# Performance work log

Hardware: AMD Instinct MI355X
Metric: run time of the kernel (lower is better)

## Reference

```python
import jax, jax.numpy as jnp
import numpy as np
from jax import lax

N_FFT = 512
HOP = 128
Q = N_FFT // HOP  # 4
KW = 2 * N_FFT - 1  # conv kernel width 1023


def _hann_periodic(n: int) -> np.ndarray:
    # scipy.signal.get_window('hann', n) default fftbins=True -> periodic hann
    k = np.arange(n)
    return (0.5 - 0.5 * np.cos(2.0 * np.pi * k / n)).astype(np.float64)


def _compute_alpha(W: np.ndarray, S: np.ndarray) -> np.ndarray:
    # Faithful port of ConsistencyLoss._compute_alpha (paper eq. 9)
    N, R = N_FFT, HOP
    alpha = np.zeros((2 * Q - 1, 2 * N - 1), dtype=np.complex64)
    for qi, q in enumerate(range(-(Q - 1), Q)):
        S_sh = np.zeros(N)
        s0, s1 = max(0, -q * R), min(N, N - q * R)
        if s0 < s1:
            S_sh[s0:s1] = S[q * R + s0: q * R + s1]
        term = W * S_sh
        f = np.fft.fft(term, 2 * N - 1)
        alpha[qi] = np.fft.fftshift(f) / N
    alpha[Q - 1, N - 1] -= 1.0
    return alpha


def setup_inputs() -> dict:
    key = jax.random.key(0)
    waveform = 0.1 * jax.random.normal(key, (4, 131072), dtype=jnp.float32)
    W_np = _hann_periodic(N_FFT)
    alpha = _compute_alpha(W_np, W_np)
    return {
        "waveform": waveform,
        "window": jnp.asarray(W_np, dtype=jnp.float32),
        "alpha_real": jnp.asarray(alpha.real, dtype=jnp.float32),
        "alpha_imag": jnp.asarray(alpha.imag, dtype=jnp.float32),
    }


def _stft(waveform, window):
    # torch.stft(center=True, pad_mode='reflect', onesided=True), output (B, T, F)
    N, hop = N_FFT, HOP
    B, L = waveform.shape
    padded = jnp.pad(waveform, ((0, 0), (N // 2, N // 2)), mode="reflect")
    T = 1 + L // hop
    idx = hop * jnp.arange(T)[:, None] + jnp.arange(N)[None, :]  # (T, N)
    frames = padded[:, idx] * window  # (B, T, N)
    return jnp.fft.rfft(frames, axis=-1)  # (B, T, N//2+1) complex64


def reference(waveform, window, alpha_real, alpha_imag):
    N, hop = N_FFT, HOP
    B = waveform.shape[0]
    H = _stft(waveform, window)  # (B, T, N//2+1)
    T = H.shape[1]

    # reconstruct full two-sided spectrum: concat conj-flipped interior bins
    H_full = jnp.concatenate([H, jnp.conj(H[:, :, 1:-1][:, :, ::-1])], axis=2)  # (B, T, N)
    H_full = jnp.transpose(H_full, (0, 2, 1))  # (B, N, T)

    # fuse the phase-term einsum into the per-frequency conv kernel:
    # C[b,n,t] = sum_q phase[n,q] * (alpha[q] * H_full[b,n])(t)
    #          = (K_eff[n] * H_full[b,n])(t),  K_eff = phase @ alpha
    q_idx = jnp.arange(-(Q - 1), Q, dtype=jnp.float32)
    n_idx = jnp.arange(N, dtype=jnp.float32)
    phase = jnp.exp(1j * (2.0 * jnp.pi / N) * n_idx[:, None] * q_idx[None, :])  # (N, 2Q-1)
    alpha = alpha_real + 1j * alpha_imag  # (2Q-1, KW)
    K = phase @ alpha.astype(jnp.complex64)  # (N, KW)
    Kr, Ki = jnp.real(K), jnp.imag(K)

    # complex depthwise (groups=N) cross-correlation via real 2-channel trick
    Hri = jnp.stack([jnp.real(H_full), jnp.imag(H_full)], axis=2).reshape(B, 2 * N, T)
    kern = jnp.stack([
        jnp.stack([Kr, -Ki], axis=1),  # real output rows (N, 2, KW)
        jnp.stack([Ki, Kr], axis=1),   # imag output rows (N, 2, KW)
    ], axis=1).reshape(2 * N, 2, KW)
    out = lax.conv_general_dilated(
        Hri, kern, window_strides=(1,), padding=[(N - 1, N - 1)],
        dimension_numbers=("NCH", "OIH", "NCH"), feature_group_count=N,
    )  # (B, 2N, T)
    Cr, Ci = out[:, 0::2], out[:, 1::2]  # (B, N, T)

    loss = jnp.sum(Cr * Cr + Ci * Ci)
    return loss / (B * T)
```

## Files before the change

kernel.cpp:

```cpp
#include <hip/hip_runtime.h>
#include <math.h>

#define T_FRAMES 1025
#define TSTRIDE  1032
#define BATCH    4
#define LWAV     131072
#define KWC      1023
#define MFFT     2048
#define PI_F     3.14159265358979323846f

struct c32 { float r, i; };
__device__ __forceinline__ c32 mkc(float r, float i){ c32 z; z.r=r; z.i=i; return z; }
__device__ __forceinline__ c32 cadd(c32 a, c32 b){ return mkc(a.r+b.r, a.i+b.i); }
__device__ __forceinline__ c32 csub(c32 a, c32 b){ return mkc(a.r-b.r, a.i-b.i); }
__device__ __forceinline__ c32 cmul(c32 a, c32 b){ return mkc(a.r*b.r - a.i*b.i, a.r*b.i + a.i*b.r); }
__device__ __forceinline__ c32 cni(c32 a){ return mkc(a.i, -a.r); }
#define C8F 0.70710678118654752440f
__device__ __forceinline__ c32 c8p(c32 a){ return mkc(C8F*(a.r+a.i), C8F*(a.i-a.r)); }
__device__ __forceinline__ c32 c8m(c32 a){ return mkc(C8F*(a.i-a.r), -C8F*(a.r+a.i)); }

__device__ __forceinline__ void st2(float2* X, int p, c32 v){ X[p] = make_float2(v.r, v.i); }
__device__ __forceinline__ c32 ld2(const float2* X, int p){ float2 e = X[p]; return mkc(e.x, e.y); }

__device__ __forceinline__ int pX(int j){ return j + (j >> 5); }
__device__ __forceinline__ int pS2(int j){ return j + (j >> 4); }
__device__ __forceinline__ int rev9(int j){ return (int)(__brev((unsigned)j) >> 23); }

__device__ __forceinline__ c32 wexp(int r) {
    float s, c;
    __sincosf((float)r * (-PI_F / 1024.0f), &s, &c);
    return mkc(c, s);
}

__device__ __forceinline__ void dif8_tw(c32 y[8], c32 w3) {
    c32 w2 = cmul(w3, w3), w1 = cmul(w2, w2);
    c32 u[8], v[8], d;
    d = csub(y[0], y[4]); u[0] = cadd(y[0], y[4]); u[4] = cmul(d, w3);
    d = csub(y[1], y[5]); u[1] = cadd(y[1], y[5]); u[5] = c8p(cmul(d, w3));
    d = csub(y[2], y[6]); u[2] = cadd(y[2], y[6]); u[6] = cni(cmul(d, w3));
    d = csub(y[3], y[7]); u[3] = cadd(y[3], y[7]); u[7] = c8m(cmul(d, w3));
    d = csub(u[0], u[2]); v[0] = cadd(u[0], u[2]); v[2] = cmul(d, w2);
    d = csub(u[1], u[3]); v[1] = cadd(u[1], u[3]); v[3] = cni(cmul(d, w2));
    d = csub(u[4], u[6]); v[4] = cadd(u[4], u[6]); v[6] = cmul(d, w2);
    d = csub(u[5], u[7]); v[5] = cadd(u[5], u[7]); v[7] = cni(cmul(d, w2));
    d = csub(v[0], v[1]); y[0] = cadd(v[0], v[1]); y[1] = cmul(d, w1);
    d = csub(v[2], v[3]); y[2] = cadd(v[2], v[3]); y[3] = cmul(d, w1);
    d = csub(v[4], v[5]); y[4] = cadd(v[4], v[5]); y[5] = cmul(d, w1);
    d = csub(v[6], v[7]); y[6] = cadd(v[6], v[7]); y[7] = cmul(d, w1);
}
__device__ __forceinline__ void dif8_nt(c32 y[8]) {
    c32 u[8], v[8], d;
    d = csub(y[0], y[4]); u[0] = cadd(y[0], y[4]); u[4] = d;
    d = csub(y[1], y[5]); u[1] = cadd(y[1], y[5]); u[5] = c8p(d);
    d = csub(y[2], y[6]); u[2] = cadd(y[2], y[6]); u[6] = cni(d);
    d = csub(y[3], y[7]); u[3] = cadd(y[3], y[7]); u[7] = c8m(d);
    d = csub(u[0], u[2]); v[0] = cadd(u[0], u[2]); v[2] = d;
    d = csub(u[1], u[3]); v[1] = cadd(u[1], u[3]); v[3] = cni(d);
    d = csub(u[4], u[6]); v[4] = cadd(u[4], u[6]); v[6] = d;
    d = csub(u[5], u[7]); v[5] = cadd(u[5], u[7]); v[7] = cni(d);
    d = csub(v[0], v[1]); y[0] = cadd(v[0], v[1]); y[1] = d;
    d = csub(v[2], v[3]); y[2] = cadd(v[2], v[3]); y[3] = d;
    d = csub(v[4], v[5]); y[4] = cadd(v[4], v[5]); y[5] = d;
    d = csub(v[6], v[7]); y[6] = cadd(v[6], v[7]); y[7] = d;
}
__device__ __forceinline__ void dit8_tw(c32 y[8], c32 w3) {
    c32 w2 = cmul(w3, w3), w1 = cmul(w2, w2);
    c32 u[8], v[8], t;
    t = cmul(y[1], w1); u[0] = cadd(y[0], t); u[1] = csub(y[0], t);
    t = cmul(y[3], w1); u[2] = cadd(y[2], t); u[3] = csub(y[2], t);
    t = cmul(y[5], w1); u[4] = cadd(y[4], t); u[5] = csub(y[4], t);
    t = cmul(y[7], w1); u[6] = cadd(y[6], t); u[7] = csub(y[6], t);
    t = cmul(u[2], w2);      v[0] = cadd(u[0], t); v[2] = csub(u[0], t);
    t = cni(cmul(u[3], w2)); v[1] = cadd(u[1], t); v[3] = csub(u[1], t);
    t = cmul(u[6], w2);      v[4] = cadd(u[4], t); v[6] = csub(u[4], t);
    t = cni(cmul(u[7], w2)); v[5] = cadd(u[5], t); v[7] = csub(u[5], t);
    t = cmul(v[4], w3);      y[0] = cadd(v[0], t); y[4] = csub(v[0], t);
    t = c8p(cmul(v[5], w3)); y[1] = cadd(v[1], t); y[5] = csub(v[1], t);
    t = cni(cmul(v[6], w3)); y[2] = cadd(v[2], t); y[6] = csub(v[2], t);
    t = c8m(cmul(v[7], w3)); y[3] = cadd(v[3], t); y[7] = csub(v[3], t);
}
__device__ __forceinline__ void dit8_nt(c32 y[8]) {
    c32 u[8], v[8], t;
    u[0] = cadd(y[0], y[1]); u[1] = csub(y[0], y[1]);
    u[2] = cadd(y[2], y[3]); u[3] = csub(y[2], y[3]);
    u[4] = cadd(y[4], y[5]); u[5] = csub(y[4], y[5]);
    u[6] = cadd(y[6], y[7]); u[7] = csub(y[6], y[7]);
    t = u[2];      v[0] = cadd(u[0], t); v[2] = csub(u[0], t);
    t = cni(u[3]); v[1] = cadd(u[1], t); v[3] = csub(u[1], t);
    t = u[6];      v[4] = cadd(u[4], t); v[6] = csub(u[4], t);
    t = cni(u[7]); v[5] = cadd(u[5], t); v[7] = csub(u[5], t);
    t = v[4];      y[0] = cadd(v[0], t); y[4] = csub(v[0], t);
    t = c8p(v[5]); y[1] = cadd(v[1], t); y[5] = csub(v[1], t);
    t = cni(v[6]); y[2] = cadd(v[2], t); y[6] = csub(v[2], t);
    t = c8m(v[7]); y[3] = cadd(v[3], t); y[7] = csub(v[3], t);
}
__device__ __forceinline__ void dif4(c32 y[4]) {
    c32 u0 = cadd(y[0], y[2]), d0 = csub(y[0], y[2]);
    c32 u1 = cadd(y[1], y[3]), d1 = cni(csub(y[1], y[3]));
    y[0] = cadd(u0, u1); y[1] = csub(u0, u1);
    y[2] = cadd(d0, d1); y[3] = csub(d0, d1);
}
__device__ __forceinline__ void dif4_tw(c32 y[4], c32 w) {
    c32 w2 = cmul(w, w), w3 = cmul(w2, w);
    c32 s0 = cadd(y[0], y[2]), d0 = csub(y[0], y[2]);
    c32 s1 = cadd(y[1], y[3]), d1 = cni(csub(y[1], y[3]));
    y[0] = cadd(s0, s1);
    y[1] = cmul(csub(s0, s1), w2);
    y[2] = cmul(cadd(d0, d1), w);
    y[3] = cmul(csub(d0, d1), w3);
}
__device__ __forceinline__ void dit4(c32 y[4], c32 w) {
    c32 w2 = cmul(w, w);
    c32 t1 = cmul(y[1], w2); c32 u0 = cadd(y[0], t1), u1 = csub(y[0], t1);
    c32 t3 = cmul(y[3], w2); c32 u2 = cadd(y[2], t3), u3 = csub(y[2], t3);
    c32 s2 = cmul(u2, w);      y[0] = cadd(u0, s2); y[2] = csub(u0, s2);
    c32 s3 = cni(cmul(u3, w)); y[1] = cadd(u1, s3); y[3] = csub(u1, s3);
}

#define FSTR 548
__global__ __launch_bounds__(256) void stage1_kernel(const float* __restrict__ wave,
                                                     const float* __restrict__ win,
                                                     const float* __restrict__ ar,
                                                     const float* __restrict__ ai,
                                                     float2* __restrict__ Ht,
                                                     float2* __restrict__ Afbr,
                                                     float* __restrict__ out) {
    __shared__ float2 S2[2192];
    const int tid = threadIdx.x;

    if (blockIdx.x >= 8) {
        float2* F = S2;
        const int bid = blockIdx.x - 8;
        const int w = tid >> 6, l = tid & 63;
        const int b = bid / 257;
        const int t0 = (bid - b * 257) << 2;
        const float* wb = wave + (size_t)b * LWAV;
        const int j = w;
        const int t = t0 + j;

#pragma unroll 1
        for (int rep = 0; rep < 2; ++rep) {
            if (t < T_FRAMES) {
                c32 y[8];
#pragma unroll
                for (int k = 0; k < 8; ++k) {
                    int s = l + (k << 6);
                    int posn = t * 128 + s - 256;
                    int ix = posn < 0 ? -posn : (posn >= LWAV ? 2 * LWAV - 2 - posn : posn);
                    y[k] = mkc(wb[ix] * win[s], 0.f);
                }
                dif8_tw(y, wexp(l << 2));
#pragma unroll
                for (int k = 0; k < 8; ++k) st2(F, j*FSTR + pS2(l + (k << 6)), y[k]);
                __builtin_amdgcn_wave_barrier();
                {
                    int base = ((l >> 3) << 6) + (l & 7);
#pragma unroll
                    for (int k = 0; k < 8; ++k) y[k] = ld2(F, j*FSTR + pS2(base + (k << 3)));
                    dif8_tw(y, wexp((l & 7) << 5));
#pragma unroll
                    for (int k = 0; k < 8; ++k) st2(F, j*FSTR + pS2(base + (k << 3)), y[k]);
                }
                __builtin_amdgcn_wave_barrier();
                {
#pragma unroll
                    for (int k = 0; k < 8; ++k) y[k] = ld2(F, j*FSTR + pS2((l << 3) + k));
                    dif8_nt(y);
#pragma unroll
                    for (int k = 0; k < 8; ++k) st2(F, j*FSTR + pS2((l << 3) + k), y[k]);
                }
            }
            __syncthreads();
            const int jj = tid & 3;
            const int rb = tid >> 2;
            if (t0 + jj < T_FRAMES) {
#pragma unroll
                for (int rr = 0; rr < 4; ++rr) {
                    int p = ((rr << 6) + rb) << 1;
                    Ht[(size_t)(b * 512 + p) * TSTRIDE + t0 + jj] = F[jj*FSTR + pS2(p)];
                }
                if (tid < 4)
                    Ht[(size_t)(b * 512 + 1) * TSTRIDE + t0 + jj] = F[jj*FSTR + pS2(1)];
            }
            __syncthreads();
        }
    } else if (blockIdx.x < 7) {
        float2* X = S2;
        const int q = blockIdx.x;
#pragma unroll 1
        for (int rep = 0; rep < 2; ++rep) {
            c32 y[8];
#pragma unroll
            for (int k = 0; k < 8; ++k) {
                int j = tid + (k << 8);
                y[k] = (j < KWC) ? mkc(ar[q * KWC + j], -ai[q * KWC + j]) : mkc(0.f, 0.f);
            }
            dif8_tw(y, wexp(tid));
#pragma unroll
            for (int k = 0; k < 8; ++k) st2(X, pX(tid + (k << 8)), y[k]);
            __syncthreads();
            {
                int base = ((tid >> 5) << 8) + (tid & 31);
#pragma unroll
                for (int k = 0; k < 8; ++k) y[k] = ld2(X, pX(base + (k << 5)));
                dif8_tw(y, wexp((tid & 31) << 3));
#pragma unroll
                for (int k = 0; k < 8; ++k) st2(X, pX(base + (k << 5)), y[k]);
            }
            __syncthreads();
            {
                int base = ((tid & 63) << 5) + (tid >> 6);
#pragma unroll
                for (int k = 0; k < 8; ++k) y[k] = ld2(X, pX(base + (k << 2)));
                dif8_tw(y, wexp((tid >> 6) << 6));
#pragma unroll
                for (int k = 0; k < 8; ++k) st2(X, pX(base + (k << 2)), y[k]);
            }
            __syncthreads();
#pragma unroll
            for (int h = 0; h < 2; ++h) {
                int g = tid + (h << 8);
                c32 z4[4];
#pragma unroll
                for (int k = 0; k < 4; ++k) z4[k] = ld2(X, pX((g << 2) + k));
                dif4(z4);
#pragma unroll
                for (int k = 0; k < 4; ++k) {
                    int jx = (g << 2) + k;
                    int j4 = jx >> 1, lo = jx & 1;
                    int wv4 = j4 >> 8, rem = j4 & 255;
                    int r = rem >> 5, c = (rem >> 2) & 7, kk = rem & 3;
                    int s = (wv4 << 8) | (kk << 6) | (r << 3) | c;
                    Afbr[(q << 11) + (s << 1) + lo] = make_float2(z4[k].r, -z4[k].i);
                }
            }
            __syncthreads();
        }
    } else {
        if (tid == 0) *out = 0.f;
    }
}

__global__ __launch_bounds__(256) void conv_kernel(const float2* __restrict__ Ht,
                                                   const float2* __restrict__ Afbr,
                                                   float* __restrict__ out) {
    __shared__ float2 S2[4224];
    __shared__ float red[4];
    const int tid = threadIdx.x;
    const int l = tid & 63, wv = tid >> 6;
    const int g = blockIdx.x;
    const int half = g / 257;
    const int n = g - half * 257;
    const int b0 = half << 1;
    const int pr = rev9(n);

    const c32 wA  = wexp(tid);
    const c32 wB  = wexp((l & 31) << 3);
    const c32 wP3 = wexp((l & 7) << 5);
    const c32 wI2 = wexp((l & 3) << 6);
    const c32 wg1B = c8p(wB);
    const c32 wg1I = c8p(wI2);
    const c32 p1 = wexp(-(n << 2));
    const c32 p2 = cmul(p1, p1);
    const c32 p3 = cmul(p2, p1);

    const int Bb   = (((wv << 1) + (l >> 5)) << 8) + (l & 31);
    const int chunk = wv << 9;
    const int p3b  = chunk + ((l >> 3) << 6) + (l & 7);
    const int pos0 = chunk + ((l >> 3) << 6) + ((l & 7) << 3);
    const int px0  = pX(pos0);
    const int i2b  = chunk + ((l >> 2) << 5) + (l & 3);
    const int i3b  = chunk + ((l >> 5) << 8) + (l & 31);
    const int abase = (wv << 8) + l;
    const float4* af4 = (const float4*)Afbr;

#pragma unroll 1
    for (int r = 0; r < 2; ++r) {
        const float2* row = Ht + (size_t)((b0 + r) * 512 + pr) * TSTRIDE;
        float2* X = S2 + r * 2112;
        c32 y[8];
#pragma unroll
        for (int k = 0; k < 4; ++k) { float2 h = row[tid + (k << 8)]; y[k] = mkc(h.x, h.y); }
        if (tid == 0) { float2 h = row[1024]; y[4] = mkc(h.x, h.y); } else y[4] = mkc(0.f, 0.f);
        y[5] = mkc(0.f, 0.f); y[6] = mkc(0.f, 0.f); y[7] = mkc(0.f, 0.f);
        dif8_tw(y, wA);
#pragma unroll
        for (int k = 0; k < 8; ++k) st2(X, pX(tid + (k << 8)), y[k]);
    }
    __syncthreads();

#pragma unroll 1
    for (int r = 0; r < 2; ++r) {
        float2* X = S2 + r * 2112;
        c32 y[8];
#pragma unroll
        for (int gg = 0; gg < 2; ++gg)
#pragma unroll
            for (int t = 0; t < 4; ++t) y[gg*4+t] = ld2(X, pX(Bb + (gg << 5) + (t << 6)));
        dif4_tw(&y[0], wB); dif4_tw(&y[4], wg1B);
#pragma unroll
        for (int gg = 0; gg < 2; ++gg)
#pragma unroll
            for (int t = 0; t < 4; ++t) st2(X, pX(Bb + (gg << 5) + (t << 6)), y[gg*4+t]);
    }
    __builtin_amdgcn_wave_barrier();

#pragma unroll 1
    for (int r = 0; r < 2; ++r) {
        float2* X = S2 + r * 2112;
        c32 y[8];
#pragma unroll
        for (int u = 0; u < 8; ++u) y[u] = ld2(X, pX(p3b + (u << 3)));
        dif8_tw(y, wP3);
#pragma unroll
        for (int u = 0; u < 8; ++u) st2(X, pX(p3b + (u << 3)), y[u]);
    }
    __builtin_amdgcn_wave_barrier();

#pragma unroll 1
    for (int r = 0; r < 2; ++r) {
        float2* X = S2 + r * 2112;
        c32 y[8];
#pragma unroll
        for (int u = 0; u < 8; ++u) y[u] = ld2(X, px0 + u);
        dif8_nt(y);
#pragma unroll
        for (int k = 0; k < 8; ++k) {
            const int kk = k >> 1;
            float4 a;
            c32 Kk;
            a = af4[(3 << 10) + abase + (kk << 6)];
            float ax = (k & 1) ? a.z : a.x, ay = (k & 1) ? a.w : a.y;
            Kk = mkc(ax, ay);
            a = af4[(4 << 10) + abase + (kk << 6)]; ax = (k & 1) ? a.z : a.x; ay = (k & 1) ? a.w : a.y;
            Kk.r += p1.r * ax - p1.i * ay;  Kk.i += p1.r * ay + p1.i * ax;
            a = af4[(2 << 10) + abase + (kk << 6)]; ax = (k & 1) ? a.z : a.x; ay = (k & 1) ? a.w : a.y;
            Kk.r += p1.r * ax + p1.i * ay;  Kk.i += p1.r * ay - p1.i * ax;
            a = af4[(5 << 10) + abase + (kk << 6)]; ax = (k & 1) ? a.z : a.x; ay = (k & 1) ? a.w : a.y;
            Kk.r += p2.r * ax - p2.i * ay;  Kk.i += p2.r * ay + p2.i * ax;
            a = af4[(1 << 10) + abase + (kk << 6)]; ax = (k & 1) ? a.z : a.x; ay = (k & 1) ? a.w : a.y;
            Kk.r += p2.r * ax + p2.i * ay;  Kk.i += p2.r * ay - p2.i * ax;
            a = af4[(6 << 10) + abase + (kk << 6)]; ax = (k & 1) ? a.z : a.x; ay = (k & 1) ? a.w : a.y;
            Kk.r += p3.r * ax - p3.i * ay;  Kk.i += p3.r * ay + p3.i * ax;
            a = af4[(0 << 10) + abase + (kk << 6)]; ax = (k & 1) ? a.z : a.x; ay = (k & 1) ? a.w : a.y;
            Kk.r += p3.r * ax + p3.i * ay;  Kk.i += p3.r * ay - p3.i * ax;
            c32 P = cmul(y[k], Kk);
            y[k] = mkc(P.r, -P.i);
        }
        dit8_nt(y);
#pragma unroll
        for (int u = 0; u < 8; ++u) st2(X, px0 + u, y[u]);
    }
    __builtin_amdgcn_wave_barrier();

#pragma unroll 1
    for (int r = 0; r < 2; ++r) {
        float2* X = S2 + r * 2112;
        c32 y[8];
#pragma unroll
        for (int gg = 0; gg < 2; ++gg)
#pragma unroll
            for (int t = 0; t < 4; ++t) y[gg*4+t] = ld2(X, pX(i2b + (gg << 2) + (t << 3)));
        dit4(&y[0], wI2); dit4(&y[4], wg1I);
#pragma unroll
        for (int gg = 0; gg < 2; ++gg)
#pragma unroll
            for (int t = 0; t < 4; ++t) st2(X, pX(i2b + (gg << 2) + (t << 3)), y[gg*4+t]);
    }
    __builtin_amdgcn_wave_barrier();

#pragma unroll 1
    for (int r = 0; r < 2; ++r) {
        float2* X = S2 + r * 2112;
        c32 y[8];
#pragma unroll
        for (int k = 0; k < 8; ++k) y[k] = ld2(X, pX(i3b + (k << 5)));
        dit8_tw(y, wB);
#pragma unroll
        for (int k = 0; k < 8; ++k) st2(X, pX(i3b + (k << 5)), y[k]);
    }
    __syncthreads();

    float local = 0.f;
#pragma unroll 1
    for (int r = 0; r < 2; ++r) {
        float2* X = S2 + r * 2112;
        c32 y[8];
#pragma unroll
        for (int k = 0; k < 8; ++k) y[k] = ld2(X, pX(tid + (k << 8)));
        dit8_tw(y, wA);
        local += y[0].r*y[0].r + y[0].i*y[0].i
               + y[1].r*y[1].r + y[1].i*y[1].i
               + y[7].r*y[7].r + y[7].i*y[7].i;
        if (tid < 2)  local += y[2].r*y[2].r + y[2].i*y[2].i;
        if (tid >= 1) local += y[6].r*y[6].r + y[6].i*y[6].i;
    }
    local *= (n == 0 || n == 256) ? 1.0f : 2.0f;
#pragma unroll
    for (int off = 32; off >= 1; off >>= 1) local += __shfl_down(local, off);
    if ((tid & 63) == 0) red[tid >> 6] = local;
    __syncthreads();
    if (tid == 0) {
        const float SCALE =
            (float)(1.0 / ((double)MFFT * (double)MFFT * (double)BATCH * (double)T_FRAMES));
        atomicAdd(out, (red[0] + red[1] + red[2] + red[3]) * SCALE);
    }
}

extern "C" void kernel_launch(void* const* d_in, const int* in_sizes, int n_in,
                              void* d_out, int out_size, void* d_ws, size_t ws_size,
                              hipStream_t stream) {
    (void)in_sizes; (void)n_in; (void)out_size; (void)ws_size;
    const float* wave   = (const float*)d_in[0];
    const float* window = (const float*)d_in[1];
    const float* ar     = (const float*)d_in[2];
    const float* ai     = (const float*)d_in[3];
    float* out = (float*)d_out;

    char* ws = (char*)d_ws;
    float2* Ht   = (float2*)ws;
    float2* Afbr = (float2*)(ws + 16908288);

    stage1_kernel<<<1036, 256, 0, stream>>>(wave, window, ar, ai, Ht, Afbr, out);
    conv_kernel<<<2 * 257, 256, 0, stream>>>(Ht, Afbr, out);
}
```

Measured before the change: 89.42 us.

## Drop duplicated stage1 repetition and give each conv block one batch row

The stage1 STFT and alpha-FFT paths each ran their whole body twice in a `rep` loop, repeating identical work; the loop is removed so each runs once. The conv kernel no longer processes two batch rows per block in a double-sized shared buffer. It now launches one block per (batch, frequency) pair, doubling the grid and halving shared memory per block to raise occupancy and parallelism. In exchange, per-block setup such as twiddle factors is repeated across more blocks.

New measurement: 88.04 us. Within noise of the previous version (-1.5%).

```diff
diff --git a/kernel.cpp b/kernel.cpp
--- a/kernel.cpp
+++ b/kernel.cpp
@@ -138,103 +138,95 @@
         const int j = w;
         const int t = t0 + j;
 
-#pragma unroll 1
-        for (int rep = 0; rep < 2; ++rep) {
-            if (t < T_FRAMES) {
-                c32 y[8];
-#pragma unroll
-                for (int k = 0; k < 8; ++k) {
-                    int s = l + (k << 6);
-                    int posn = t * 128 + s - 256;
-                    int ix = posn < 0 ? -posn : (posn >= LWAV ? 2 * LWAV - 2 - posn : posn);
-                    y[k] = mkc(wb[ix] * win[s], 0.f);
-                }
-                dif8_tw(y, wexp(l << 2));
-#pragma unroll
-                for (int k = 0; k < 8; ++k) st2(F, j*FSTR + pS2(l + (k << 6)), y[k]);
-                __builtin_amdgcn_wave_barrier();
-                {
-                    int base = ((l >> 3) << 6) + (l & 7);
-#pragma unroll
-                    for (int k = 0; k < 8; ++k) y[k] = ld2(F, j*FSTR + pS2(base + (k << 3)));
-                    dif8_tw(y, wexp((l & 7) << 5));
-#pragma unroll
-                    for (int k = 0; k < 8; ++k) st2(F, j*FSTR + pS2(base + (k << 3)), y[k]);
-                }
-                __builtin_amdgcn_wave_barrier();
-                {
-#pragma unroll
-                    for (int k = 0; k < 8; ++k) y[k] = ld2(F, j*FSTR + pS2((l << 3) + k));
-                    dif8_nt(y);
-#pragma unroll
-                    for (int k = 0; k < 8; ++k) st2(F, j*FSTR + pS2((l << 3) + k), y[k]);
-                }
-            }
-            __syncthreads();
-            const int jj = tid & 3;
-            const int rb = tid >> 2;
-            if (t0 + jj < T_FRAMES) {
-#pragma unroll
-                for (int rr = 0; rr < 4; ++rr) {
-                    int p = ((rr << 6) + rb) << 1;
-                    Ht[(size_t)(b * 512 + p) * TSTRIDE + t0 + jj] = F[jj*FSTR + pS2(p)];
-                }
-                if (tid < 4)
-                    Ht[(size_t)(b * 512 + 1) * TSTRIDE + t0 + jj] = F[jj*FSTR + pS2(1)];
-            }
-            __syncthreads();
+        if (t < T_FRAMES) {
+            c32 y[8];
+#pragma unroll
+            for (int k = 0; k < 8; ++k) {
+                int s = l + (k << 6);
+                int posn = t * 128 + s - 256;
+                int ix = posn < 0 ? -posn : (posn >= LWAV ? 2 * LWAV - 2 - posn : posn);
+                y[k] = mkc(wb[ix] * win[s], 0.f);
+            }
+            dif8_tw(y, wexp(l << 2));
+#pragma unroll
+            for (int k = 0; k < 8; ++k) st2(F, j*FSTR + pS2(l + (k << 6)), y[k]);
+            __builtin_amdgcn_wave_barrier();
+            {
+                int base = ((l >> 3) << 6) + (l & 7);
+#pragma unroll
+                for (int k = 0; k < 8; ++k) y[k] = ld2(F, j*FSTR + pS2(base + (k << 3)));
+                dif8_tw(y, wexp((l & 7) << 5));
+#pragma unroll
+                for (int k = 0; k < 8; ++k) st2(F, j*FSTR + pS2(base + (k << 3)), y[k]);
+            }
+            __builtin_amdgcn_wave_barrier();
+            {
+#pragma unroll
+                for (int k = 0; k < 8; ++k) y[k] = ld2(F, j*FSTR + pS2((l << 3) + k));
+                dif8_nt(y);
+#pragma unroll
+                for (int k = 0; k < 8; ++k) st2(F, j*FSTR + pS2((l << 3) + k), y[k]);
+            }
+        }
+        __syncthreads();
+        const int jj = tid & 3;
+        const int rb = tid >> 2;
+        if (t0 + jj < T_FRAMES) {
+#pragma unroll
+            for (int rr = 0; rr < 4; ++rr) {
+                int p = ((rr << 6) + rb) << 1;
+                Ht[(size_t)(b * 512 + p) * TSTRIDE + t0 + jj] = F[jj*FSTR + pS2(p)];
+            }
+            if (tid < 4)
+                Ht[(size_t)(b * 512 + 1) * TSTRIDE + t0 + jj] = F[jj*FSTR + pS2(1)];
         }
     } else if (blockIdx.x < 7) {
         float2* X = S2;
         const int q = blockIdx.x;
-#pragma unroll 1
-        for (int rep = 0; rep < 2; ++rep) {
-            c32 y[8];
-#pragma unroll
-            for (int k = 0; k < 8; ++k) {
-                int j = tid + (k << 8);
-                y[k] = (j < KWC) ? mkc(ar[q * KWC + j], -ai[q * KWC + j]) : mkc(0.f, 0.f);
-            }
-            dif8_tw(y, wexp(tid));
-#pragma unroll
-            for (int k = 0; k < 8; ++k) st2(X, pX(tid + (k << 8)), y[k]);
-            __syncthreads();
-            {
-                int base = ((tid >> 5) << 8) + (tid & 31);
-#pragma unroll
-                for (int k = 0; k < 8; ++k) y[k] = ld2(X, pX(base + (k << 5)));
-                dif8_tw(y, wexp((tid & 31) << 3));
-#pragma unroll
-                for (int k = 0; k < 8; ++k) st2(X, pX(base + (k << 5)), y[k]);
-            }
-            __syncthreads();
-            {
-                int base = ((tid & 63) << 5) + (tid >> 6);
-#pragma unroll
-                for (int k = 0; k < 8; ++k) y[k] = ld2(X, pX(base + (k << 2)));
-                dif8_tw(y, wexp((tid >> 6) << 6));
-#pragma unroll
-                for (int k = 0; k < 8; ++k) st2(X, pX(base + (k << 2)), y[k]);
-            }
-            __syncthreads();
-#pragma unroll
-            for (int h = 0; h < 2; ++h) {
-                int g = tid + (h << 8);
-                c32 z4[4];
-#pragma unroll
-                for (int k = 0; k < 4; ++k) z4[k] = ld2(X, pX((g << 2) + k));
-                dif4(z4);
-#pragma unroll
-                for (int k = 0; k < 4; ++k) {
-                    int jx = (g << 2) + k;
-                    int j4 = jx >> 1, lo = jx & 1;
-                    int wv4 = j4 >> 8, rem = j4 & 255;
-                    int r = rem >> 5, c = (rem >> 2) & 7, kk = rem & 3;
-                    int s = (wv4 << 8) | (kk << 6) | (r << 3) | c;
-                    Afbr[(q << 11) + (s << 1) + lo] = make_float2(z4[k].r, -z4[k].i);
-                }
-            }
-            __syncthreads();
+        c32 y[8];
+#pragma unroll
+        for (int k = 0; k < 8; ++k) {
+            int j = tid + (k << 8);
+            y[k] = (j < KWC) ? mkc(ar[q * KWC + j], -ai[q * KWC + j]) : mkc(0.f, 0.f);
+        }
+        dif8_tw(y, wexp(tid));
+#pragma unroll
+        for (int k = 0; k < 8; ++k) st2(X, pX(tid + (k << 8)), y[k]);
+        __syncthreads();
+        {
+            int base = ((tid >> 5) << 8) + (tid & 31);
+#pragma unroll
+            for (int k = 0; k < 8; ++k) y[k] = ld2(X, pX(base + (k << 5)));
+            dif8_tw(y, wexp((tid & 31) << 3));
+#pragma unroll
+            for (int k = 0; k < 8; ++k) st2(X, pX(base + (k << 5)), y[k]);
+        }
+        __syncthreads();
+        {
+            int base = ((tid & 63) << 5) + (tid >> 6);
+#pragma unroll
+            for (int k = 0; k < 8; ++k) y[k] = ld2(X, pX(base + (k << 2)));
+            dif8_tw(y, wexp((tid >> 6) << 6));
+#pragma unroll
+            for (int k = 0; k < 8; ++k) st2(X, pX(base + (k << 2)), y[k]);
+        }
+        __syncthreads();
+#pragma unroll
+        for (int h = 0; h < 2; ++h) {
+            int g = tid + (h << 8);
+            c32 z4[4];
+#pragma unroll
+            for (int k = 0; k < 4; ++k) z4[k] = ld2(X, pX((g << 2) + k));
+            dif4(z4);
+#pragma unroll
+            for (int k = 0; k < 4; ++k) {
+                int jx = (g << 2) + k;
+                int j4 = jx >> 1, lo = jx & 1;
+                int wv4 = j4 >> 8, rem = j4 & 255;
+                int r = rem >> 5, c = (rem >> 2) & 7, kk = rem & 3;
+                int s = (wv4 << 8) | (kk << 6) | (r << 3) | c;
+                Afbr[(q << 11) + (s << 1) + lo] = make_float2(z4[k].r, -z4[k].i);
+            }
         }
     } else {
         if (tid == 0) *out = 0.f;
@@ -244,15 +236,15 @@
 __global__ __launch_bounds__(256) void conv_kernel(const float2* __restrict__ Ht,
                                                    const float2* __restrict__ Afbr,
                                                    float* __restrict__ out) {
-    __shared__ float2 S2[4224];
+    __shared__ float2 X[2112];
     __shared__ float red[4];
     const int tid = threadIdx.x;
     const int l = tid & 63, wv = tid >> 6;
     const int g = blockIdx.x;
-    const int half = g / 257;
-    const int n = g - half * 257;
-    const int b0 = half << 1;
+    const int b = g / 257;
+    const int n = g - b * 257;
     const int pr = rev9(n);
+    const float2* row = Ht + (size_t)(b * 512 + pr) * TSTRIDE;
 
     const c32 wA  = wexp(tid);
     const c32 wB  = wexp((l & 31) << 3);
@@ -274,127 +266,92 @@
     const int abase = (wv << 8) + l;
     const float4* af4 = (const float4*)Afbr;
 
-#pragma unroll 1
-    for (int r = 0; r < 2; ++r) {
-        const float2* row = Ht + (size_t)((b0 + r) * 512 + pr) * TSTRIDE;
-        float2* X = S2 + r * 2112;
-        c32 y[8];
-#pragma unroll
-        for (int k = 0; k < 4; ++k) { float2 h = row[tid + (k << 8)]; y[k] = mkc(h.x, h.y); }
-        if (tid == 0) { float2 h = row[1024]; y[4] = mkc(h.x, h.y); } else y[4] = mkc(0.f, 0.f);
-        y[5] = mkc(0.f, 0.f); y[6] = mkc(0.f, 0.f); y[7] = mkc(0.f, 0.f);
-        dif8_tw(y, wA);
-#pragma unroll
-        for (int k = 0; k < 8; ++k) st2(X, pX(tid + (k << 8)), y[k]);
+    c32 y[8];
+#pragma unroll
+    for (int k = 0; k < 4; ++k) { float2 h = row[tid + (k << 8)]; y[k] = mkc(h.x, h.y); }
+    if (tid == 0) { float2 h = row[1024]; y[4] = mkc(h.x, h.y); } else y[4] = mkc(0.f, 0.f);
+    y[5] = mkc(0.f, 0.f); y[6] = mkc(0.f, 0.f); y[7] = mkc(0.f, 0.f);
+    dif8_tw(y, wA);
+#pragma unroll
+    for (int k = 0; k < 8; ++k) st2(X, pX(tid + (k << 8)), y[k]);
+    __syncthreads();
+
+#pragma unroll
+    for (int gg = 0; gg < 2; ++gg)
+#pragma unroll
+        for (int t = 0; t < 4; ++t) y[gg*4+t] = ld2(X, pX(Bb + (gg << 5) + (t << 6)));
+    dif4_tw(&y[0], wB); dif4_tw(&y[4], wg1B);
+#pragma unroll
+    for (int gg = 0; gg < 2; ++gg)
+#pragma unroll
+        for (int t = 0; t < 4; ++t) st2(X, pX(Bb + (gg << 5) + (t << 6)), y[gg*4+t]);
+    __builtin_amdgcn_wave_barrier();
+
+#pragma unroll
+    for (int u = 0; u < 8; ++u) y[u] = ld2(X, pX(p3b + (u << 3)));
+    dif8_tw(y, wP3);
+#pragma unroll
+    for (int u = 0; u < 8; ++u) st2(X, pX(p3b + (u << 3)), y[u]);
+    __builtin_amdgcn_wave_barrier();
+
+#pragma unroll
+    for (int u = 0; u < 8; ++u) y[u] = ld2(X, px0 + u);
+    dif8_nt(y);
+#pragma unroll
+    for (int k = 0; k < 8; ++k) {
+        const int kk = k >> 1;
+        float4 a;
+        c32 Kk;
+        a = af4[(3 << 10) + abase + (kk << 6)];
+        float ax = (k & 1) ? a.z : a.x, ay = (k & 1) ? a.w : a.y;
+        Kk = mkc(ax, ay);
+        a = af4[(4 << 10) + abase + (kk << 6)]; ax = (k & 1) ? a.z : a.x; ay = (k & 1) ? a.w : a.y;
+        Kk.r += p1.r * ax - p1.i * ay;  Kk.i += p1.r * ay + p1.i * ax;
+        a = af4[(2 << 10) + abase + (kk << 6)]; ax = (k & 1) ? a.z : a.x; ay = (k & 1) ? a.w : a.y;
+        Kk.r += p1.r * ax + p1.i * ay;  Kk.i += p1.r * ay - p1.i * ax;
+        a = af4[(5 << 10) + abase + (kk << 6)]; ax = (k & 1) ? a.z : a.x; ay = (k & 1) ? a.w : a.y;
+        Kk.r += p2.r * ax - p2.i * ay;  Kk.i += p2.r * ay + p2.i * ax;
+        a = af4[(1 << 10) + abase + (kk << 6)]; ax = (k & 1) ? a.z : a.x; ay = (k & 1) ? a.w : a.y;
+        Kk.r += p2.r * ax + p2.i * ay;  Kk.i += p2.r * ay - p2.i * ax;
+        a = af4[(6 << 10) + abase + (kk << 6)]; ax = (k & 1) ? a.z : a.x; ay = (k & 1) ? a.w : a.y;
+        Kk.r += p3.r * ax - p3.i * ay;  Kk.i += p3.r * ay + p3.i * ax;
+        a = af4[(0 << 10) + abase + (kk << 6)]; ax = (k & 1) ? a.z : a.x; ay = (k & 1) ? a.w : a.y;
+        Kk.r += p3.r * ax + p3.i * ay;  Kk.i += p3.r * ay - p3.i * ax;
+        c32 P = cmul(y[k], Kk);
+        y[k] = mkc(P.r, -P.i);
     }
+    dit8_nt(y);
+#pragma unroll
+    for (int u = 0; u < 8; ++u) st2(X, px0 + u, y[u]);
+    __builtin_amdgcn_wave_barrier();
+
+#pragma unroll
+    for (int gg = 0; gg < 2; ++gg)
+#pragma unroll
+        for (int t = 0; t < 4; ++t) y[gg*4+t] = ld2(X, pX(i2b + (gg << 2) + (t << 3)));
+    dit4(&y[0], wI2); dit4(&y[4], wg1I);
+#pragma unroll
+    for (int gg = 0; gg < 2; ++gg)
+#pragma unroll
+        for (int t = 0; t < 4; ++t) st2(X, pX(i2b + (gg << 2) + (t << 3)), y[gg*4+t]);
+    __builtin_amdgcn_wave_barrier();
+
+#pragma unroll
+    for (int k = 0; k < 8; ++k) y[k] = ld2(X, pX(i3b + (k << 5)));
+    dit8_tw(y, wB);
+#pragma unroll
+    for (int k = 0; k < 8; ++k) st2(X, pX(i3b + (k << 5)), y[k]);
     __syncthreads();
 
-#pragma unroll 1
-    for (int r = 0; r < 2; ++r) {
-        float2* X = S2 + r * 2112;
-        c32 y[8];
-#pragma unroll
-        for (int gg = 0; gg < 2; ++gg)
-#pragma unroll
-            for (int t = 0; t < 4; ++t) y[gg*4+t] = ld2(X, pX(Bb + (gg << 5) + (t << 6)));
-        dif4_tw(&y[0], wB); dif4_tw(&y[4], wg1B);
-#pragma unroll
-        for (int gg = 0; gg < 2; ++gg)
-#pragma unroll
-            for (int t = 0; t < 4; ++t) st2(X, pX(Bb + (gg << 5) + (t << 6)), y[gg*4+t]);
-    }
-    __builtin_amdgcn_wave_barrier();
-
-#pragma unroll 1
-    for (int r = 0; r < 2; ++r) {
-        float2* X = S2 + r * 2112;
-        c32 y[8];
-#pragma unroll
-        for (int u = 0; u < 8; ++u) y[u] = ld2(X, pX(p3b + (u << 3)));
-        dif8_tw(y, wP3);
-#pragma unroll
-        for (int u = 0; u < 8; ++u) st2(X, pX(p3b + (u << 3)), y[u]);
-    }
-    __builtin_amdgcn_wave_barrier();
-
-#pragma unroll 1
-    for (int r = 0; r < 2; ++r) {
-        float2* X = S2 + r * 2112;
-        c32 y[8];
-#pragma unroll
-        for (int u = 0; u < 8; ++u) y[u] = ld2(X, px0 + u);
-        dif8_nt(y);
-#pragma unroll
-        for (int k = 0; k < 8; ++k) {
-            const int kk = k >> 1;
-            float4 a;
-            c32 Kk;
-            a = af4[(3 << 10) + abase + (kk << 6)];
-            float ax = (k & 1) ? a.z : a.x, ay = (k & 1) ? a.w : a.y;
-            Kk = mkc(ax, ay);
-            a = af4[(4 << 10) + abase + (kk << 6)]; ax = (k & 1) ? a.z : a.x; ay = (k & 1) ? a.w : a.y;
-            Kk.r += p1.r * ax - p1.i * ay;  Kk.i += p1.r * ay + p1.i * ax;
-            a = af4[(2 << 10) + abase + (kk << 6)]; ax = (k & 1) ? a.z : a.x; ay = (k & 1) ? a.w : a.y;
-            Kk.r += p1.r * ax + p1.i * ay;  Kk.i += p1.r * ay - p1.i * ax;
-            a = af4[(5 << 10) + abase + (kk << 6)]; ax = (k & 1) ? a.z : a.x; ay = (k & 1) ? a.w : a.y;
-            Kk.r += p2.r * ax - p2.i * ay;  Kk.i += p2.r * ay + p2.i * ax;
-            a = af4[(1 << 10) + abase + (kk << 6)]; ax = (k & 1) ? a.z : a.x; ay = (k & 1) ? a.w : a.y;
-            Kk.r += p2.r * ax + p2.i * ay;  Kk.i += p2.r * ay - p2.i * ax;
-            a = af4[(6 << 10) + abase + (kk << 6)]; ax = (k & 1) ? a.z : a.x; ay = (k & 1) ? a.w : a.y;
-            Kk.r += p3.r * ax - p3.i * ay;  Kk.i += p3.r * ay + p3.i * ax;
-            a = af4[(0 << 10) + abase + (kk << 6)]; ax = (k & 1) ? a.z : a.x; ay = (k & 1) ? a.w : a.y;
-            Kk.r += p3.r * ax + p3.i * ay;  Kk.i += p3.r * ay - p3.i * ax;
-            c32 P = cmul(y[k], Kk);
-            y[k] = mkc(P.r, -P.i);
-        }
-        dit8_nt(y);
-#pragma unroll
-        for (int u = 0; u < 8; ++u) st2(X, px0 + u, y[u]);
-    }
-    __builtin_amdgcn_wave_barrier();
-
-#pragma unroll 1
-    for (int r = 0; r < 2; ++r) {
-        float2* X = S2 + r * 2112;
-        c32 y[8];
-#pragma unroll
-        for (int gg = 0; gg < 2; ++gg)
-#pragma unroll
-            for (int t = 0; t < 4; ++t) y[gg*4+t] = ld2(X, pX(i2b + (gg << 2) + (t << 3)));
-        dit4(&y[0], wI2); dit4(&y[4], wg1I);
-#pragma unroll
-        for (int gg = 0; gg < 2; ++gg)
-#pragma unroll
-            for (int t = 0; t < 4; ++t) st2(X, pX(i2b + (gg << 2) + (t << 3)), y[gg*4+t]);
-    }
-    __builtin_amdgcn_wave_barrier();
-
-#pragma unroll 1
-    for (int r = 0; r < 2; ++r) {
-        float2* X = S2 + r * 2112;
-        c32 y[8];
-#pragma unroll
-        for (int k = 0; k < 8; ++k) y[k] = ld2(X, pX(i3b + (k << 5)));
-        dit8_tw(y, wB);
-#pragma unroll
-        for (int k = 0; k < 8; ++k) st2(X, pX(i3b + (k << 5)), y[k]);
-    }
-    __syncthreads();
-
-    float local = 0.f;
-#pragma unroll 1
-    for (int r = 0; r < 2; ++r) {
-        float2* X = S2 + r * 2112;
-        c32 y[8];
-#pragma unroll
-        for (int k = 0; k < 8; ++k) y[k] = ld2(X, pX(tid + (k << 8)));
-        dit8_tw(y, wA);
-        local += y[0].r*y[0].r + y[0].i*y[0].i
-               + y[1].r*y[1].r + y[1].i*y[1].i
-               + y[7].r*y[7].r + y[7].i*y[7].i;
-        if (tid < 2)  local += y[2].r*y[2].r + y[2].i*y[2].i;
-        if (tid >= 1) local += y[6].r*y[6].r + y[6].i*y[6].i;
-    }
+#pragma unroll
+    for (int k = 0; k < 8; ++k) y[k] = ld2(X, pX(tid + (k << 8)));
+    dit8_tw(y, wA);
+    float local = y[0].r*y[0].r + y[0].i*y[0].i
+                + y[1].r*y[1].r + y[1].i*y[1].i
+                + y[7].r*y[7].r + y[7].i*y[7].i;
+    if (tid < 2)  local += y[2].r*y[2].r + y[2].i*y[2].i;
+    if (tid >= 1) local += y[6].r*y[6].r + y[6].i*y[6].i;
+
     local *= (n == 0 || n == 256) ? 1.0f : 2.0f;
 #pragma unroll
     for (int off = 32; off >= 1; off >>= 1) local += __shfl_down(local, off);
@@ -422,5 +379,5 @@
     float2* Afbr = (float2*)(ws + 16908288);
 
     stage1_kernel<<<1036, 256, 0, stream>>>(wave, window, ar, ai, Ht, Afbr, out);
-    conv_kernel<<<2 * 257, 256, 0, stream>>>(Ht, Afbr, out);
-}
+    conv_kernel<<<4 * 257, 256, 0, stream>>>(Ht, Afbr, out);
+}
```
